# Performance work log

Hardware: AMD Instinct MI355X
Metric: run time of the kernel (lower is better)

The kernel has to match this reference:

```python
import jax, jax.numpy as jnp
import numpy as np

N_WAY = 5
K_SHOT = 5
TEMPERATURE = 0.2
EPS = 1e-12  # torch F.normalize eps


def setup_inputs() -> dict:
    key = jax.random.key(0)
    k1, k2, k3, k4 = jax.random.split(key, 4)
    b, q, c, h, w = 4, 75, 640, 10, 10
    s = N_WAY * K_SHOT
    return {
        "support_xf": jax.random.normal(k1, (b, s, c, h, w), dtype=jnp.float32),
        "support_y": jax.random.randint(k2, (b, s), 0, N_WAY),
        "query_xf": jax.random.normal(k3, (b, q, c, h, w), dtype=jnp.float32),
        "query_y": jax.random.randint(k4, (b, q), 0, N_WAY),
    }


def _l2norm(x):
    # normalize along last axis (channel), matching F.normalize semantics
    n = jnp.sqrt(jnp.sum(x * x, axis=-1, keepdims=True))
    return x / jnp.maximum(n, EPS)


def _inner_simi(support_xf, query_xf):
    # cosine similarity between all query local descriptors and all support
    # local descriptors, grouped per class -> [b, q, N, M_q, M_s]
    b, s, c, h, w = support_xf.shape
    q = query_xf.shape[1]
    hw = h * w
    Ms = K_SHOT * hw
    sx = support_xf.reshape(b, N_WAY, K_SHOT, c, hw)
    sx = jnp.transpose(sx, (0, 1, 2, 4, 3)).reshape(b, N_WAY, Ms, c)  # [b,N,M_s,c]
    qx = jnp.transpose(query_xf.reshape(b, q, c, hw), (0, 1, 3, 2))  # [b,q,M_q,c]
    return jnp.einsum('bqmc,bnsc->bqnms', _l2norm(qx), _l2norm(sx))


def _dmnn_mask(simi):
    # simi: [b,q,N,M_q,M_s] -> bool mask [b,q,M_q]
    b, q, N, Mq, Ms = simi.shape
    merged = jnp.transpose(simi, (0, 1, 3, 2, 4)).reshape(b, q, Mq, N * Ms)
    query_nearest = jnp.argmax(merged, axis=-1)            # [b,q,M_q] global NN idx
    class_max = jnp.max(simi, axis=-1)                      # [b,q,N,M_q]
    top2 = jax.lax.top_k(jnp.transpose(class_max, (0, 1, 3, 2)), 2)[0]  # [b,q,M_q,2]
    query_class_diff = top2[..., 0] - top2[..., 1]          # [b,q,M_q]
    diffs_m = jax.nn.one_hot(query_nearest, N * Ms, dtype=simi.dtype) \
        * query_class_diff[..., None]                       # [b,q,M_q,N*M_s]
    diffs_max_nearest = jnp.argmax(diffs_m, axis=-2)        # [b,q,N*M_s]
    gathered = jnp.take_along_axis(diffs_max_nearest, query_nearest, axis=-1)  # [b,q,M_q]
    return gathered == jnp.arange(Mq)[None, None, :]


def reference(support_xf, support_y, query_xf, query_y):
    b, q = query_xf.shape[0], query_xf.shape[1]
    simi = _inner_simi(support_xf, query_xf)                # [b,q,N,M_q,M_s]
    q_mask = _dmnn_mask(simi)                               # [b,q,M_q]
    class_max = jnp.max(simi, axis=-1)                      # [b,q,N,M_q]
    query_value = jnp.sum(class_max * q_mask[:, :, None, :].astype(simi.dtype), axis=-1)
    logits = query_value.reshape(b * q, N_WAY) / TEMPERATURE
    logp = jax.nn.log_softmax(logits, axis=-1)
    labels = query_y.reshape(b * q)
    loss = -jnp.mean(jnp.take_along_axis(logp, labels[:, None], axis=1))
    return loss
```

## Files before the change

kernel.cpp:

```cpp
#include <hip/hip_runtime.h>
#include <math.h>

#define B 4
#define Q 75
#define NBQ (B*Q)
#define NWAY 5
#define KSHOT 5
#define C 640
#define HW 100
#define MS 500
#define SLAB (C*HW)

#define MT64_B 118
#define RT_B 472
#define A_CHUNKS_B (RT_B*20*64)
#define S_CHUNKS_ALL (20*32*20*64)
#define S_CHUNKS_B   (5*32*20*64)

#define CHI 0.00390625f
#define CLO 1.9073486328125e-06f

typedef _Float16 half8 __attribute__((ext_vector_type(8)));
typedef float f32x4 __attribute__((ext_vector_type(4)));

__device__ __forceinline__ void gl_lds16(const void* gsrc, void* ldst) {
  __builtin_amdgcn_global_load_lds(
      (const __attribute__((address_space(1))) unsigned int*)gsrc,
      (__attribute__((address_space(3))) unsigned int*)ldst, 16, 0, 0);
}

#define WS_BASE 340352ull
#define NEED_ALL   104908288ull
#define NEED_PERB   46908928ull
#define NEED_PERB2  27248128ull

__global__ __launch_bounds__(256) void norm_kernel(const float* __restrict__ s_xf,
                                                   const float* __restrict__ q_xf,
                                                   float* __restrict__ invs,
                                                   float* __restrict__ invq) {
  int id = blockIdx.x;
  const float* base;
  float* out;
  if (id < 100) { base = s_xf + (size_t)id * SLAB;        out = invs + id * HW; }
  else          { base = q_xf + (size_t)(id - 100) * SLAB; out = invq + (id - 100) * HW; }
  __shared__ float ssum[2][HW];
  int t = threadIdx.x;
  if (t < 2 * HW) ((float*)ssum)[t] = 0.f;
  __syncthreads();
  if (t < 2 * HW) {
    int p = t % HW, half = t / HW;
    float part = 0.f;
    for (int ch = half * 320; ch < half * 320 + 320; ++ch) {
      float v = base[ch * HW + p];
      part = fmaf(v, v, part);
    }
    ssum[half][p] = part;
  }
  __syncthreads();
  if (t < HW) {
    float nrm = sqrtf(ssum[0][t] + ssum[1][t]);
    out[t] = 1.f / fmaxf(nrm, 1e-12f);
  }
}

__device__ __forceinline__ void dual_split(float w, _Float16* h0, _Float16* h1) {
  _Float16 a = (_Float16)w;
  *h0 = a;
  *h1 = (_Float16)((w - (float)a) * 2048.f);
}

__global__ __launch_bounds__(256) void convs_kernel(const float* __restrict__ s_xf,
                                                    const float* __restrict__ invs,
                                                    uint4* __restrict__ o0,
                                                    uint4* __restrict__ o1,
                                                    int bn0) {
  int id = blockIdx.x * 256 + threadIdx.x;
  int lane = id & 63;
  int tmp = id >> 6;
  int ks = tmp % 20;
  int t2 = tmp / 20;
  int jf = t2 % 32;
  int bnl = t2 / 32;
  int bn = bn0 + bnl;
  int j = jf * 16 + (lane & 15);
  int k = ks * 32 + (lane >> 4) * 8;
  union { _Float16 h[8]; uint4 u; } p0, p1;
  if (j < MS) {
    int s = j / 100, p = j % 100;
    int slab = bn * 5 + s;
    const float* src = s_xf + ((size_t)slab * 640 + k) * 100 + p;
    float sc = invs[slab * 100 + p] * 16.f;
#pragma unroll
    for (int kj = 0; kj < 8; ++kj)
      dual_split(src[kj * 100] * sc, &p0.h[kj], &p1.h[kj]);
  } else {
    p0.u = make_uint4(0, 0, 0, 0);
    p1.u = make_uint4(0, 0, 0, 0);
  }
  o0[id] = p0.u; o1[id] = p1.u;
}

__global__ __launch_bounds__(256) void convq_kernel(const float* __restrict__ q_xf,
                                                    const float* __restrict__ invq,
                                                    uint4* __restrict__ o0,
                                                    uint4* __restrict__ o1,
                                                    int b0) {
  int id = blockIdx.x * 256 + threadIdx.x;
  int bloc = id / A_CHUNKS_B;
  int c = id % A_CHUNKS_B;
  int bb = b0 + bloc;
  int lane = c & 63;
  int tmp = c >> 6;
  int ks = tmp % 20;
  int rt = tmp / 20;
  int row = rt * 16 + (lane & 15);
  int k = ks * 32 + (lane >> 4) * 8;
  union { _Float16 h[8]; uint4 u; } p0, p1;
  if (row < Q * HW) {
    int qi = row / 100, p = row % 100;
    const float* src = q_xf + ((size_t)(bb * Q + qi) * 640 + k) * 100 + p;
    float sc = invq[(bb * Q + qi) * 100 + p] * 16.f;
#pragma unroll
    for (int kj = 0; kj < 8; ++kj)
      dual_split(src[kj * 100] * sc, &p0.h[kj], &p1.h[kj]);
  } else {
    p0.u = make_uint4(0, 0, 0, 0);
    p1.u = make_uint4(0, 0, 0, 0);
  }
  o0[id] = p0.u; o1[id] = p1.u;
}

__global__ __launch_bounds__(256, 2) void gemm_kernel(
    const uint4* __restrict__ a0, const uint4* __restrict__ a1,
    const uint4* __restrict__ b0p, const uint4* __restrict__ b1p,
    float* __restrict__ cmax, int* __restrict__ carg,
    int bq0, int aStride, int sbnBase, int mode ) {
  int wgid = blockIdx.x;
  int x = wgid & 7, s = wgid >> 3;
  int o;
  if (mode == 0) {
    o = x * 295 + s;
  } else {
    if (x < 6) { if (s >= 74) return; o = x * 74 + s; }
    else       { if (s >= 73) return; o = 444 + (x - 6) * 73 + s; }
  }
  int bnloc = o / MT64_B;
  int mt64 = o % MT64_B;
  int bloc = bnloc / 5;
  int n = bnloc % 5;
  int bb = bq0 + bloc;
  const uint4* A0 = a0 + (size_t)bloc * aStride;
  const uint4* A1 = a1 + (size_t)bloc * aStride;
  int bnl = bb * 5 + n - sbnBase;

  __shared__ __align__(16) _Float16 sA[2][2][4][512];
  __shared__ float sV[4][64];
  __shared__ int   sJ[4][64];

  int t = threadIdx.x;
  int w = t >> 6, lane = t & 63;

  ((float*)sV)[t] = -1e30f;
  ((int*)sJ)[t] = 0;

#define STAGE_A1(KS, BUF) do {                                                  \
    size_t aIdx = ((size_t)(mt64 * 4 + w) * 20 + (KS)) * 64 + lane;             \
    gl_lds16(A0 + aIdx, (void*)&sA[(BUF)][0][w][0]);                            \
    gl_lds16(A1 + aIdx, (void*)&sA[(BUF)][1][w][0]);                            \
  } while (0)

  for (int pass = 0; pass < 2; ++pass) {
    int jf0 = pass * 16 + w * 4;
    size_t bBase = (size_t)(bnl * 32 + jf0) * 1280 + lane;

    f32x4 acc0[4][4], accM[4][4];
#pragma unroll
    for (int mf = 0; mf < 4; ++mf)
#pragma unroll
      for (int f = 0; f < 4; ++f) {
        acc0[mf][f] = (f32x4){0.f, 0.f, 0.f, 0.f};
        accM[mf][f] = (f32x4){0.f, 0.f, 0.f, 0.f};
      }

    STAGE_A1(0, 0);
    for (int ks = 0; ks < 20; ++ks) {
      int cur = ks & 1;
      __syncthreads();

      size_t bo = bBase + (size_t)ks * 64;
      half8 bv0[4], bv1[4];
#pragma unroll
      for (int f = 0; f < 4; ++f) bv0[f] = *(const half8*)&b0p[bo + (size_t)f * 1280];
#pragma unroll
      for (int f = 0; f < 4; ++f) bv1[f] = *(const half8*)&b1p[bo + (size_t)f * 1280];
      __builtin_amdgcn_sched_barrier(0);

      if (ks < 19) STAGE_A1(ks + 1, cur ^ 1);
      __builtin_amdgcn_sched_barrier(0);

#pragma unroll
      for (int mf = 0; mf < 4; ++mf) {
        half8 av0 = *(const half8*)&sA[cur][0][mf][lane * 8];
        half8 av1 = *(const half8*)&sA[cur][1][mf][lane * 8];
#pragma unroll
        for (int f = 0; f < 4; ++f) {
          acc0[mf][f] = __builtin_amdgcn_mfma_f32_16x16x32_f16(av0, bv0[f], acc0[mf][f], 0, 0, 0);
          accM[mf][f] = __builtin_amdgcn_mfma_f32_16x16x32_f16(av0, bv1[f], accM[mf][f], 0, 0, 0);
          accM[mf][f] = __builtin_amdgcn_mfma_f32_16x16x32_f16(av1, bv0[f], accM[mf][f], 0, 0, 0);
        }
      }
    }

#pragma unroll
    for (int mf = 0; mf < 4; ++mf)
#pragma unroll
      for (int f = 0; f < 4; ++f) {
        int j = pass * 256 + w * 64 + f * 16 + (lane & 15);
        bool ok = (j < MS);
#pragma unroll
        for (int rg = 0; rg < 4; ++rg) {
          float v = ok ? (acc0[mf][f][rg] * CHI + accM[mf][f][rg] * CLO) : -1e30f;
          int ji = ok ? j : 0x7fffffff;
#pragma unroll
          for (int mk = 1; mk < 16; mk <<= 1) {
            float ov = __shfl_xor(v, mk);
            int oj = __shfl_xor(ji, mk);
            if (ov > v || (ov == v && oj < ji)) { v = ov; ji = oj; }
          }
          if ((lane & 15) == 0) {
            int row64 = mf * 16 + (lane >> 4) * 4 + rg;
            if (v > sV[w][row64]) { sV[w][row64] = v; sJ[w][row64] = ji; }
          }
        }
      }
  }
#undef STAGE_A1

  __syncthreads();
  if (w == 0) {
    int row64 = lane;
    float v = sV[0][row64];
    int ji = sJ[0][row64];
#pragma unroll
    for (int q4 = 1; q4 < 4; ++q4) {
      float ov = sV[q4][row64];
      int oj = sJ[q4][row64];
      if (ov > v || (ov == v && oj < ji)) { v = ov; ji = oj; }
    }
    int r = mt64 * 64 + row64;
    if (r < Q * HW) {
      int bq = bb * Q + r / 100, p = r % 100;
      size_t oo = (size_t)(bq * NWAY + n) * HW + p;
      cmax[oo] = v;
      carg[oo] = ji;
    }
  }
}

#define TCF 32
#define TJF 64
__global__ __launch_bounds__(256) void simi_kernel(const float* __restrict__ s_xf,
                                                   const float* __restrict__ q_xf,
                                                   const float* __restrict__ invs,
                                                   const float* __restrict__ invq,
                                                   float* __restrict__ cmax,
                                                   int* __restrict__ carg) {
  int id = blockIdx.x;
  int n = id % NWAY;
  int bq = id / NWAY;
  int b = bq / Q;
  const float* qbase = q_xf + (size_t)bq * SLAB;
  const float* sbase = s_xf + (size_t)(b * 25 + n * KSHOT) * SLAB;
  const float* invqB = invq + bq * HW;
  const float* invsB = invs + (b * 2500 + n * MS);

  __shared__ __align__(16) float As[TCF][112];
  __shared__ __align__(16) float Bs[TCF][TJF];
  __shared__ float sInvQ[HW];
  __shared__ float sInvS[MS];

  int t = threadIdx.x;
  for (int i = t; i < HW; i += 256) sInvQ[i] = invqB[i];
  for (int i = t; i < MS; i += 256) sInvS[i] = invsB[i];

  int tj = t & 15, tm = t >> 4;
  float best[7];
  int bidx[7];
#pragma unroll
  for (int r = 0; r < 7; ++r) { best[r] = -1e30f; bidx[r] = 0; }

  for (int jt0 = 0; jt0 < MS; jt0 += TJF) {
    float acc[7][4];
#pragma unroll
    for (int r = 0; r < 7; ++r)
#pragma unroll
      for (int jj = 0; jj < 4; ++jj) acc[r][jj] = 0.f;
    for (int c0 = 0; c0 < C; c0 += TCF) {
      __syncthreads();
      for (int i = t; i < TCF * HW; i += 256) {
        int p = i % HW;
        As[i / HW][p] = qbase[c0 * HW + i] * sInvQ[p];
      }
      for (int i = t; i < TCF * TJF; i += 256) {
        int cc = i / TJF, jj = i % TJF;
        int j = jt0 + jj;
        float v = 0.f;
        if (j < MS) v = sbase[(j / 100) * SLAB + (c0 + cc) * 100 + (j % 100)] * sInvS[j];
        Bs[cc][jj] = v;
      }
      __syncthreads();
#pragma unroll
      for (int cc = 0; cc < TCF; ++cc) {
        float4 bv = *(const float4*)&Bs[cc][tj * 4];
#pragma unroll
        for (int r = 0; r < 7; ++r) {
          float a = As[cc][tm * 7 + r];
          acc[r][0] = fmaf(a, bv.x, acc[r][0]);
          acc[r][1] = fmaf(a, bv.y, acc[r][1]);
          acc[r][2] = fmaf(a, bv.z, acc[r][2]);
          acc[r][3] = fmaf(a, bv.w, acc[r][3]);
        }
      }
    }
#pragma unroll
    for (int r = 0; r < 7; ++r)
#pragma unroll
      for (int jj = 0; jj < 4; ++jj) {
        int j = jt0 + tj * 4 + jj;
        float v = acc[r][jj];
        if (j < MS && v > best[r]) { best[r] = v; bidx[r] = j; }
      }
  }
#pragma unroll
  for (int r = 0; r < 7; ++r)
#pragma unroll
    for (int mask = 1; mask < 16; mask <<= 1) {
      float ov = __shfl_xor(best[r], mask);
      int oi = __shfl_xor(bidx[r], mask);
      if (ov > best[r] || (ov == best[r] && oi < bidx[r])) { best[r] = ov; bidx[r] = oi; }
    }
  if (tj == 0)
#pragma unroll
    for (int r = 0; r < 7; ++r) {
      int m = tm * 7 + r;
      if (m < HW) {
        cmax[(size_t)(bq * NWAY + n) * HW + m] = best[r];
        carg[(size_t)(bq * NWAY + n) * HW + m] = bidx[r];
      }
    }
}

__global__ __launch_bounds__(128) void mask_loss_kernel(const float* __restrict__ cmax,
                                                        const int* __restrict__ carg,
                                                        const int* __restrict__ query_y,
                                                        float* __restrict__ lossv) {
  int bq = blockIdx.x;
  int t = threadIdx.x;
  __shared__ float sDiff[HW];
  __shared__ int sNear[HW];
  __shared__ float sCm[NWAY][HW];
  __shared__ float red[128];

  if (t < HW) {
    float cm[NWAY];
#pragma unroll
    for (int nn = 0; nn < NWAY; ++nn) {
      cm[nn] = cmax[(size_t)(bq * NWAY + nn) * HW + t];
      sCm[nn][t] = cm[nn];
    }
    float v0 = -1e30f, v1 = -1e30f;
#pragma unroll
    for (int nn = 0; nn < NWAY; ++nn) {
      float v = cm[nn];
      if (v > v0) { v1 = v0; v0 = v; }
      else if (v > v1) { v1 = v; }
    }
    sDiff[t] = v0 - v1;
    float gb = -1e30f;
    int gn = 0;
#pragma unroll
    for (int nn = 0; nn < NWAY; ++nn)
      if (cm[nn] > gb) { gb = cm[nn]; gn = nn; }
    sNear[t] = gn * MS + carg[(size_t)(bq * NWAY + gn) * HW + t];
  }
  __syncthreads();

  bool msk = false;
  if (t < HW) {
    int j = sNear[t];
    int wn = 0;
    float wv = -1.f;
    for (int mp = 0; mp < HW; ++mp) {
      float v = (sNear[mp] == j) ? sDiff[mp] : 0.f;
      if (v > wv) { wv = v; wn = mp; }
    }
    msk = (wn == t);
  }

  float qv[NWAY];
#pragma unroll
  for (int nn = 0; nn < NWAY; ++nn) {
    __syncthreads();
    red[t] = (t < HW && msk) ? sCm[nn][t] : 0.f;
    __syncthreads();
    for (int s = 64; s > 0; s >>= 1) {
      if (t < s) red[t] += red[t + s];
      __syncthreads();
    }
    qv[nn] = red[0];
  }

  if (t == 0) {
    float logits[NWAY], mx = -1e30f;
#pragma unroll
    for (int nn = 0; nn < NWAY; ++nn) {
      logits[nn] = qv[nn] / 0.2f;
      mx = fmaxf(mx, logits[nn]);
    }
    float se = 0.f;
#pragma unroll
    for (int nn = 0; nn < NWAY; ++nn) se += expf(logits[nn] - mx);
    float lse = mx + logf(se);
    int label = query_y[bq];
    lossv[bq] = -(logits[label] - lse);
  }
}

__global__ __launch_bounds__(512) void finalize_kernel(const float* __restrict__ lossv,
                                                       float* __restrict__ out) {
  __shared__ float red[512];
  int t = threadIdx.x;
  red[t] = (t < NBQ) ? lossv[t] : 0.f;
  __syncthreads();
  for (int s = 256; s > 0; s >>= 1) {
    if (t < s) red[t] += red[t + s];
    __syncthreads();
  }
  if (t == 0) out[0] = red[0] / (float)NBQ;
}

extern "C" void kernel_launch(void* const* d_in, const int* in_sizes, int n_in,
                              void* d_out, int out_size, void* d_ws, size_t ws_size,
                              hipStream_t stream) {
  const float* s_xf = (const float*)d_in[0];
  const float* q_xf = (const float*)d_in[2];
  const int* query_y = (const int*)d_in[3];

  float* ws = (float*)d_ws;
  float* invs = ws;
  float* invq = ws + 10000;
  float* cmax = ws + 40000;
  int* carg = (int*)(ws + 190000);
  float* lossv = ws + 340000;

  norm_kernel<<<400, 256, 0, stream>>>(s_xf, q_xf, invs, invq);

  const size_t SP_ALL = 3276800, SP_B = 819200, QS_B = 2416640;

  if (ws_size >= NEED_ALL) {
    uint4* S0 = (uint4*)(ws + WS_BASE);
    uint4* S1 = (uint4*)(ws + WS_BASE + SP_ALL);
    uint4* Q0 = (uint4*)(ws + WS_BASE + 2 * SP_ALL);
    uint4* Q1 = (uint4*)(ws + WS_BASE + 2 * SP_ALL + 4 * QS_B);
    convs_kernel<<<S_CHUNKS_ALL / 256, 256, 0, stream>>>(s_xf, invs, S0, S1, 0);
    convq_kernel<<<4 * A_CHUNKS_B / 256, 256, 0, stream>>>(q_xf, invq, Q0, Q1, 0);
    gemm_kernel<<<2360, 256, 0, stream>>>(Q0, Q1, S0, S1,
                                          cmax, carg, 0, A_CHUNKS_B, 0, 0);
  } else if (ws_size >= NEED_PERB) {
    uint4* S0 = (uint4*)(ws + WS_BASE);
    uint4* S1 = (uint4*)(ws + WS_BASE + SP_ALL);
    uint4* Q0 = (uint4*)(ws + WS_BASE + 2 * SP_ALL);
    uint4* Q1 = (uint4*)(ws + WS_BASE + 2 * SP_ALL + QS_B);
    convs_kernel<<<S_CHUNKS_ALL / 256, 256, 0, stream>>>(s_xf, invs, S0, S1, 0);
    for (int b = 0; b < 4; ++b) {
      convq_kernel<<<A_CHUNKS_B / 256, 256, 0, stream>>>(q_xf, invq, Q0, Q1, b);
      gemm_kernel<<<592, 256, 0, stream>>>(Q0, Q1, S0, S1,
                                           cmax, carg, b, 0, 0, 1);
    }
  } else if (ws_size >= NEED_PERB2) {
    uint4* S0 = (uint4*)(ws + WS_BASE);
    uint4* S1 = (uint4*)(ws + WS_BASE + SP_B);
    uint4* Q0 = (uint4*)(ws + WS_BASE + 2 * SP_B);
    uint4* Q1 = (uint4*)(ws + WS_BASE + 2 * SP_B + QS_B);
    for (int b = 0; b < 4; ++b) {
      convs_kernel<<<S_CHUNKS_B / 256, 256, 0, stream>>>(s_xf, invs, S0, S1, b * 5);
      convq_kernel<<<A_CHUNKS_B / 256, 256, 0, stream>>>(q_xf, invq, Q0, Q1, b);
      gemm_kernel<<<592, 256, 0, stream>>>(Q0, Q1, S0, S1,
                                           cmax, carg, b, 0, b * 5, 1);
    }
  } else {
    simi_kernel<<<1500, 256, 0, stream>>>(s_xf, q_xf, invs, invq, cmax, carg);
  }

  mask_loss_kernel<<<NBQ, 128, 0, stream>>>(cmax, carg, query_y, lossv);
  finalize_kernel<<<1, 512, 0, stream>>>(lossv, (float*)d_out);
}
```

Baseline: 599.6 us.

## Widen GEMM block to eight waves covering all support columns in one pass

The GEMM kernel now runs 512 threads, and its eight waves together cover all 512 support columns in a single pass. Before, four waves made two passes, so each A tile was loaded twice. A is staged in larger chunks of five k-steps with double buffering, which cuts the barrier count from 20 per pass to 4 in total. The tile-to-block mapping is also reordered so that adjacent blocks share the same query M-tile across the 20 batch-class pairs, which should improve L2 reuse of A. In exchange, LDS use is larger, the 512-thread launch bounds may limit registers, and per-k-step B loads are no longer overlapped with A staging through the explicit schedule barriers.

```diff
diff --git a/kernel.cpp b/kernel.cpp
--- a/kernel.cpp
+++ b/kernel.cpp
@@ -130,7 +130,7 @@
   o0[id] = p0.u; o1[id] = p1.u;
 }
 
-__global__ __launch_bounds__(256, 2) void gemm_kernel(
+__global__ __launch_bounds__(512, 2) void gemm_kernel(
     const uint4* __restrict__ a0, const uint4* __restrict__ a1,
     const uint4* __restrict__ b0p, const uint4* __restrict__ b1p,
     float* __restrict__ cmax, int* __restrict__ carg,
@@ -144,64 +144,66 @@
     if (x < 6) { if (s >= 74) return; o = x * 74 + s; }
     else       { if (s >= 73) return; o = 444 + (x - 6) * 73 + s; }
   }
-  int bnloc = o / MT64_B;
-  int mt64 = o % MT64_B;
-  int bloc = bnloc / 5;
-  int n = bnloc % 5;
+  int mt64, bloc, n;
+  if (mode == 0) { mt64 = o / 20; int bn = o % 20; bloc = bn / 5; n = bn % 5; }
+  else           { mt64 = o / 5;  n = o % 5;       bloc = 0; }
   int bb = bq0 + bloc;
   const uint4* A0 = a0 + (size_t)bloc * aStride;
   const uint4* A1 = a1 + (size_t)bloc * aStride;
   int bnl = bb * 5 + n - sbnBase;
 
-  __shared__ __align__(16) _Float16 sA[2][2][4][512];
-  __shared__ float sV[4][64];
-  __shared__ int   sJ[4][64];
+  __shared__ __align__(16) _Float16 sA[2][2][5][4][512];
+  __shared__ float sV[8][64];
+  __shared__ int   sJ[8][64];
 
   int t = threadIdx.x;
   int w = t >> 6, lane = t & 63;
 
-  ((float*)sV)[t] = -1e30f;
-  ((int*)sJ)[t] = 0;
-
-#define STAGE_A1(KS, BUF) do {                                                  \
-    size_t aIdx = ((size_t)(mt64 * 4 + w) * 20 + (KS)) * 64 + lane;             \
-    gl_lds16(A0 + aIdx, (void*)&sA[(BUF)][0][w][0]);                            \
-    gl_lds16(A1 + aIdx, (void*)&sA[(BUF)][1][w][0]);                            \
+  sV[w][lane] = -1e30f;
+  sJ[w][lane] = 0;
+
+#define STAGE_C(CH, BUF) do {                                                   \
+    _Pragma("unroll")                                                           \
+    for (int q = 0; q < 5; ++q) {                                               \
+      int idx = w * 5 + q;                                                      \
+      int limb = idx / 20, rem = idx % 20;                                      \
+      int kl = rem / 4, rtl = rem % 4;                                          \
+      size_t aIdx = ((size_t)(mt64 * 4 + rtl) * 20 + ((CH) * 5 + kl)) * 64 + lane; \
+      gl_lds16((limb ? A1 : A0) + aIdx, (void*)&sA[(BUF)][limb][kl][rtl][0]);   \
+    }                                                                           \
   } while (0)
 
-  for (int pass = 0; pass < 2; ++pass) {
-    int jf0 = pass * 16 + w * 4;
-    size_t bBase = (size_t)(bnl * 32 + jf0) * 1280 + lane;
-
-    f32x4 acc0[4][4], accM[4][4];
-#pragma unroll
-    for (int mf = 0; mf < 4; ++mf)
-#pragma unroll
-      for (int f = 0; f < 4; ++f) {
-        acc0[mf][f] = (f32x4){0.f, 0.f, 0.f, 0.f};
-        accM[mf][f] = (f32x4){0.f, 0.f, 0.f, 0.f};
-      }
-
-    STAGE_A1(0, 0);
-    for (int ks = 0; ks < 20; ++ks) {
-      int cur = ks & 1;
-      __syncthreads();
-
+  size_t bBase = (size_t)(bnl * 32 + w * 4) * 1280 + lane;
+
+  f32x4 acc0[4][4], accM[4][4];
+#pragma unroll
+  for (int mf = 0; mf < 4; ++mf)
+#pragma unroll
+    for (int f = 0; f < 4; ++f) {
+      acc0[mf][f] = (f32x4){0.f, 0.f, 0.f, 0.f};
+      accM[mf][f] = (f32x4){0.f, 0.f, 0.f, 0.f};
+    }
+
+  STAGE_C(0, 0);
+  __syncthreads();
+
+  for (int c = 0; c < 4; ++c) {
+    int cur = c & 1;
+    if (c < 3) STAGE_C(c + 1, cur ^ 1);
+
+#pragma unroll
+    for (int kl = 0; kl < 5; ++kl) {
+      int ks = c * 5 + kl;
       size_t bo = bBase + (size_t)ks * 64;
       half8 bv0[4], bv1[4];
 #pragma unroll
       for (int f = 0; f < 4; ++f) bv0[f] = *(const half8*)&b0p[bo + (size_t)f * 1280];
 #pragma unroll
       for (int f = 0; f < 4; ++f) bv1[f] = *(const half8*)&b1p[bo + (size_t)f * 1280];
-      __builtin_amdgcn_sched_barrier(0);
-
-      if (ks < 19) STAGE_A1(ks + 1, cur ^ 1);
-      __builtin_amdgcn_sched_barrier(0);
-
 #pragma unroll
       for (int mf = 0; mf < 4; ++mf) {
-        half8 av0 = *(const half8*)&sA[cur][0][mf][lane * 8];
-        half8 av1 = *(const half8*)&sA[cur][1][mf][lane * 8];
+        half8 av0 = *(const half8*)&sA[cur][0][kl][mf][lane * 8];
+        half8 av1 = *(const half8*)&sA[cur][1][kl][mf][lane * 8];
 #pragma unroll
         for (int f = 0; f < 4; ++f) {
           acc0[mf][f] = __builtin_amdgcn_mfma_f32_16x16x32_f16(av0, bv0[f], acc0[mf][f], 0, 0, 0);
@@ -210,41 +212,42 @@
         }
       }
     }
-
-#pragma unroll
-    for (int mf = 0; mf < 4; ++mf)
-#pragma unroll
-      for (int f = 0; f < 4; ++f) {
-        int j = pass * 256 + w * 64 + f * 16 + (lane & 15);
-        bool ok = (j < MS);
-#pragma unroll
-        for (int rg = 0; rg < 4; ++rg) {
-          float v = ok ? (acc0[mf][f][rg] * CHI + accM[mf][f][rg] * CLO) : -1e30f;
-          int ji = ok ? j : 0x7fffffff;
-#pragma unroll
-          for (int mk = 1; mk < 16; mk <<= 1) {
-            float ov = __shfl_xor(v, mk);
-            int oj = __shfl_xor(ji, mk);
-            if (ov > v || (ov == v && oj < ji)) { v = ov; ji = oj; }
-          }
-          if ((lane & 15) == 0) {
-            int row64 = mf * 16 + (lane >> 4) * 4 + rg;
-            if (v > sV[w][row64]) { sV[w][row64] = v; sJ[w][row64] = ji; }
-          }
+    __syncthreads();
+  }
+#undef STAGE_C
+
+#pragma unroll
+  for (int mf = 0; mf < 4; ++mf)
+#pragma unroll
+    for (int f = 0; f < 4; ++f) {
+      int j = w * 64 + f * 16 + (lane & 15);
+      bool ok = (j < MS);
+#pragma unroll
+      for (int rg = 0; rg < 4; ++rg) {
+        float v = ok ? (acc0[mf][f][rg] * CHI + accM[mf][f][rg] * CLO) : -1e30f;
+        int ji = ok ? j : 0x7fffffff;
+#pragma unroll
+        for (int mk = 1; mk < 16; mk <<= 1) {
+          float ov = __shfl_xor(v, mk);
+          int oj = __shfl_xor(ji, mk);
+          if (ov > v || (ov == v && oj < ji)) { v = ov; ji = oj; }
         }
-      }
-  }
-#undef STAGE_A1
-
+        if ((lane & 15) == 0) {
+          int row64 = mf * 16 + (lane >> 4) * 4 + rg;
+          if (v > sV[w][row64]) { sV[w][row64] = v; sJ[w][row64] = ji; }
+        }
+      }
+    }
   __syncthreads();
+
   if (w == 0) {
     int row64 = lane;
     float v = sV[0][row64];
     int ji = sJ[0][row64];
 #pragma unroll
-    for (int q4 = 1; q4 < 4; ++q4) {
-      float ov = sV[q4][row64];
-      int oj = sJ[q4][row64];
+    for (int q8 = 1; q8 < 8; ++q8) {
+      float ov = sV[q8][row64];
+      int oj = sJ[q8][row64];
       if (ov > v || (ov == v && oj < ji)) { v = ov; ji = oj; }
     }
     int r = mt64 * 64 + row64;
@@ -464,7 +467,7 @@
     uint4* Q1 = (uint4*)(ws + WS_BASE + 2 * SP_ALL + 4 * QS_B);
     convs_kernel<<<S_CHUNKS_ALL / 256, 256, 0, stream>>>(s_xf, invs, S0, S1, 0);
     convq_kernel<<<4 * A_CHUNKS_B / 256, 256, 0, stream>>>(q_xf, invq, Q0, Q1, 0);
-    gemm_kernel<<<2360, 256, 0, stream>>>(Q0, Q1, S0, S1,
+    gemm_kernel<<<2360, 512, 0, stream>>>(Q0, Q1, S0, S1,
                                           cmax, carg, 0, A_CHUNKS_B, 0, 0);
   } else if (ws_size >= NEED_PERB) {
     uint4* S0 = (uint4*)(ws + WS_BASE);
@@ -474,7 +477,7 @@
     convs_kernel<<<S_CHUNKS_ALL / 256, 256, 0, stream>>>(s_xf, invs, S0, S1, 0);
     for (int b = 0; b < 4; ++b) {
       convq_kernel<<<A_CHUNKS_B / 256, 256, 0, stream>>>(q_xf, invq, Q0, Q1, b);
-      gemm_kernel<<<592, 256, 0, stream>>>(Q0, Q1, S0, S1,
+      gemm_kernel<<<592, 512, 0, stream>>>(Q0, Q1, S0, S1,
                                            cmax, carg, b, 0, 0, 1);
     }
   } else if (ws_size >= NEED_PERB2) {
@@ -485,7 +488,7 @@
     for (int b = 0; b < 4; ++b) {
       convs_kernel<<<S_CHUNKS_B / 256, 256, 0, stream>>>(s_xf, invs, S0, S1, b * 5);
       convq_kernel<<<A_CHUNKS_B / 256, 256, 0, stream>>>(q_xf, invq, Q0, Q1, b);
-      gemm_kernel<<<592, 256, 0, stream>>>(Q0, Q1, S0, S1,
+      gemm_kernel<<<592, 512, 0, stream>>>(Q0, Q1, S0, S1,
                                            cmax, carg, b, 0, b * 5, 1);
     }
   } else {
```

Measured after the change: 781.2 us. +30.3%, slower.
